# Kernel tuning notes

Hardware: AMD Instinct MI355X
Metric: run time of the kernel (lower is better)

Reference implementation:

```python
import jax, jax.numpy as jnp
import numpy as np

N_NODES = 100000
N_EDGES = 1600000
IN_FEATS = 512
HEADS = 8
HID = 8            # out_feats per head of the input layer
N_CLASSES = 40
NEG_SLOPE = 0.2    # DGL GATv2Conv default


def gatv2_layer(h, src, dst, Ws, bs, Wd, bd, attn, n_nodes):
    """One DGL-style GATv2Conv (eval mode: dropouts are identity).
    h: [N, F_in]; Ws/Wd: [F_in, H*D]; attn: [H, D]. Returns [N, H*D]."""
    H, D = attn.shape
    hs = (h @ Ws + bs).reshape(-1, H, D)   # fc_src(h)
    hd = (h @ Wd + bd).reshape(-1, H, D)   # fc_dst(h)
    es = hs[src]                           # [E,H,D] messages (feat_src on edges)
    ed = hd[dst]                           # [E,H,D]
    e = jax.nn.leaky_relu(es + ed, NEG_SLOPE)
    logits = jnp.einsum('ehd,hd->eh', e, attn)          # [E,H]
    # segment softmax over incoming edges of each dst node
    m = jax.ops.segment_max(logits, dst, num_segments=n_nodes)
    m = jnp.where(jnp.isfinite(m), m, 0.0)              # nodes with no in-edges
    p = jnp.exp(logits - m[dst])
    s = jax.ops.segment_sum(p, dst, num_segments=n_nodes)
    alpha = p / (s[dst] + 1e-9)                         # [E,H]
    out = jax.ops.segment_sum(alpha[:, :, None] * es, dst, num_segments=n_nodes)
    return out.reshape(n_nodes, H * D)


def setup_inputs() -> dict:
    key = jax.random.key(0)
    ks = jax.random.split(key, 12)
    x = jax.random.normal(ks[0], (N_NODES, IN_FEATS), dtype=jnp.float32)
    src = jax.random.randint(ks[1], (N_EDGES,), 0, N_NODES, dtype=jnp.int32)
    dst = jax.random.randint(ks[2], (N_EDGES,), 0, N_NODES, dtype=jnp.int32)
    s1 = 1.0 / np.sqrt(IN_FEATS)
    s2 = 1.0 / np.sqrt(HEADS * HID)
    W1s = jax.random.normal(ks[3], (IN_FEATS, HEADS * HID), dtype=jnp.float32) * s1
    W1d = jax.random.normal(ks[4], (IN_FEATS, HEADS * HID), dtype=jnp.float32) * s1
    b1s = jnp.zeros((HEADS * HID,), jnp.float32)
    b1d = jnp.zeros((HEADS * HID,), jnp.float32)
    a1 = jax.random.normal(ks[5], (HEADS, HID), dtype=jnp.float32) * s2
    W2s = jax.random.normal(ks[6], (HEADS * HID, N_CLASSES), dtype=jnp.float32) * s2
    W2d = jax.random.normal(ks[7], (HEADS * HID, N_CLASSES), dtype=jnp.float32) * s2
    b2s = jnp.zeros((N_CLASSES,), jnp.float32)
    b2d = jnp.zeros((N_CLASSES,), jnp.float32)
    a2 = jax.random.normal(ks[8], (1, N_CLASSES), dtype=jnp.float32) * (1.0 / np.sqrt(N_CLASSES))
    return {"x": x, "src": src, "dst": dst,
            "W1s": W1s, "b1s": b1s, "W1d": W1d, "b1d": b1d, "a1": a1,
            "W2s": W2s, "b2s": b2s, "W2d": W2d, "b2d": b2d, "a2": a2}


def reference(x, src, dst, W1s, b1s, W1d, b1d, a1, W2s, b2s, W2d, b2d, a2):
    h = gatv2_layer(x, src, dst, W1s, b1s, W1d, b1d, a1, N_NODES)   # [N, H*HID]
    h = jax.nn.elu(h)
    out = gatv2_layer(h, src, dst, W2s, b2s, W2d, b2d, a2, N_NODES)  # [N, C]
    return out
```

## Files before the change

kernel.cpp:

```cpp
#include <hip/hip_runtime.h>
#include <math.h>

#define N_NODES 100000
#define N_EDGES 1600000
#define F_IN    512
#define HD1     64
#define NHEAD   8
#define NC      40
#define NEG_SLOPE 0.2f

typedef _Float16 h8 __attribute__((ext_vector_type(8)));
typedef _Float16 h4 __attribute__((ext_vector_type(4)));
typedef float f4 __attribute__((ext_vector_type(4)));

__global__ __launch_bounds__(256) void prep_all(
    const float* __restrict__ W1s, const float* __restrict__ W1d,
    _Float16* __restrict__ btgf,
    const float* __restrict__ W2s, const float* __restrict__ W2d,
    _Float16* __restrict__ btg2, int* __restrict__ deg){
  int i = blockIdx.x*256 + threadIdx.x;
  {
    int j = i & 7, lane = (i>>3)&63, t = (i>>9)&7, kstep = i>>12;
    int k = kstep*32 + (lane>>4)*8 + j;
    int n = t*16 + (lane&15);
    float v = (n < 64) ? W1s[k*64 + n] : W1d[k*64 + (n-64)];
    btgf[i] = (_Float16)v;
  }
  if(i < 80*64){
    int n = i >> 6, k = i & 63;
    float v = (n < 40) ? W2s[k*40 + n] : W2d[k*40 + (n-40)];
    btg2[i] = (_Float16)v;
  }
  for(int k=i; k<N_NODES; k+=65536) deg[k] = 0;
}

__global__ __launch_bounds__(256,4) void gemm1_hist(
    const float* __restrict__ x, const _Float16* __restrict__ btgf,
    const float* __restrict__ bs, const float* __restrict__ bd,
    _Float16* __restrict__ hs, _Float16* __restrict__ hd,
    const int* __restrict__ dst, int* __restrict__ deg){
  __shared__ _Float16 at[2][64*136];
  int gid = blockIdx.x;
  int gdiv = gid/9;
  if(gid - gdiv*9 != 0){
    int hb = gid - gdiv - 1;
    int xcd = hb & 7;
    int lo = xcd*12500, hi = lo + 12500;
    int e0 = (hb >> 3)*1024 + threadIdx.x*4;
    if(e0 + 3 < N_EDGES){
      int4 d4 = *(const int4*)&dst[e0];
      if(d4.x >= lo && d4.x < hi) atomicAdd(&deg[d4.x], 1);
      if(d4.y >= lo && d4.y < hi) atomicAdd(&deg[d4.y], 1);
      if(d4.z >= lo && d4.z < hi) atomicAdd(&deg[d4.z], 1);
      if(d4.w >= lo && d4.w < hi) atomicAdd(&deg[d4.w], 1);
    } else {
      for(int j=0;j<4;j++){
        int e = e0 + j;
        if(e < N_EDGES){
          int d = dst[e];
          if(d >= lo && d < hi) atomicAdd(&deg[d], 1);
        }
      }
    }
    return;
  }
  int tid = threadIdx.x;
  int lane = tid & 63, w = tid >> 6;
  int l15 = lane & 15, quad = lane >> 4;
  int row0 = gdiv * 64;

  f4 acc[4][2];
  #pragma unroll
  for(int rt=0;rt<4;rt++){ acc[rt][0] = (f4){0.f,0.f,0.f,0.f}; acc[rt][1] = (f4){0.f,0.f,0.f,0.f}; }

  int sr[8], sc4[8];
  #pragma unroll
  for(int j=0;j<8;j++){
    int s = tid + j*256;
    int r = s >> 5, c4 = s & 31;
    int gr = row0 + r; if(gr >= N_NODES) gr = N_NODES-1;
    sr[j] = gr; sc4[j] = c4;
  }

  float4 pf[8];
  #pragma unroll
  for(int j=0;j<8;j++)
    pf[j] = *(const float4*)&x[sr[j]*F_IN + sc4[j]*4];

  for(int kc=0; kc<4; kc++){
    int buf = kc & 1;
    #pragma unroll
    for(int j=0;j<8;j++){
      int s = tid + j*256;
      int r = s >> 5, c4 = s & 31;
      h4 hv;
      hv[0]=(_Float16)pf[j].x; hv[1]=(_Float16)pf[j].y;
      hv[2]=(_Float16)pf[j].z; hv[3]=(_Float16)pf[j].w;
      *(h4*)&at[buf][r*136 + c4*4] = hv;
    }
    if(kc < 3){
      #pragma unroll
      for(int j=0;j<8;j++)
        pf[j] = *(const float4*)&x[sr[j]*F_IN + (kc+1)*128 + sc4[j]*4];
    }
    __syncthreads();
    #pragma unroll
    for(int ks=0;ks<4;ks++){
      int fbase = (((kc*4+ks)*8) + 2*w)*512 + lane*8;
      h8 b0 = *(const h8*)&btgf[fbase];
      h8 b1 = *(const h8*)&btgf[fbase + 512];
      #pragma unroll
      for(int rt=0;rt<4;rt++){
        h8 af = *(const h8*)&at[buf][(rt*16+l15)*136 + ks*32 + quad*8];
        acc[rt][0] = __builtin_amdgcn_mfma_f32_16x16x32_f16(af, b0, acc[rt][0], 0,0,0);
        acc[rt][1] = __builtin_amdgcn_mfma_f32_16x16x32_f16(af, b1, acc[rt][1], 0,0,0);
      }
    }
  }
  #pragma unroll
  for(int tt=0;tt<2;tt++){
    int colg = (2*w+tt)*16 + l15;
    float bv; _Float16* op; int c;
    if(colg < 64){ bv = bs[colg]; op = hs; c = colg; }
    else         { bv = bd[colg-64]; op = hd; c = colg-64; }
    #pragma unroll
    for(int rt=0;rt<4;rt++){
      #pragma unroll
      for(int reg=0;reg<4;reg++){
        int rr = row0 + rt*16 + quad*4 + reg;
        if(rr < N_NODES) op[rr*HD1 + c] = (_Float16)(acc[rt][tt][reg] + bv);
      }
    }
  }
}

__global__ __launch_bounds__(256) void scan1(const int* __restrict__ deg,
                                             int* __restrict__ row,
                                             int* __restrict__ bsum){
  __shared__ int sm[256];
  int t = threadIdx.x;
  int base = blockIdx.x*1024 + t*4;
  int v0 = base+0<N_NODES ? deg[base+0] : 0;
  int v1 = base+1<N_NODES ? deg[base+1] : 0;
  int v2 = base+2<N_NODES ? deg[base+2] : 0;
  int v3 = base+3<N_NODES ? deg[base+3] : 0;
  int tsum = v0+v1+v2+v3;
  sm[t] = tsum; __syncthreads();
  for(int off=1; off<256; off<<=1){
    int x = (t>=off) ? sm[t-off] : 0;
    __syncthreads();
    sm[t] += x;
    __syncthreads();
  }
  int excl = sm[t] - tsum;
  if(t==255) bsum[blockIdx.x] = sm[255];
  if(base+0<N_NODES) row[base+0] = excl;
  if(base+1<N_NODES) row[base+1] = excl+v0;
  if(base+2<N_NODES) row[base+2] = excl+v0+v1;
  if(base+3<N_NODES) row[base+3] = excl+v0+v1+v2;
}

#define SB_N 98
__global__ __launch_bounds__(256) void scan23(int* __restrict__ row,
                                              const int* __restrict__ bsum,
                                              int* __restrict__ cur){
  __shared__ int sm[128];
  __shared__ int sme[128];
  int t = threadIdx.x;
  int v = 0;
  if(t < 128){
    v = (t < SB_N) ? bsum[t] : 0;
    sm[t] = v;
  }
  __syncthreads();
  for(int off=1; off<128; off<<=1){
    int x = 0;
    if(t < 128 && t >= off) x = sm[t-off];
    __syncthreads();
    if(t < 128) sm[t] += x;
    __syncthreads();
  }
  if(t < 128) sme[t] = sm[t] - v;
  __syncthreads();
  int i = blockIdx.x*256 + t;
  if(i < N_NODES){
    int r = row[i] + sme[i>>10];
    row[i] = r; cur[i] = r;
  }
}

__global__ __launch_bounds__(256) void scatter_edges(const int* __restrict__ src,
                                                     const int* __restrict__ dst,
                                                     int* __restrict__ cur,
                                                     int* __restrict__ esrc){
  int xcd = blockIdx.x & 7;
  int lo = xcd*12500, hi = lo + 12500;
  int e0 = (blockIdx.x >> 3)*1024 + threadIdx.x*4;
  if(e0 + 3 < N_EDGES){
    int4 d4 = *(const int4*)&dst[e0];
    int4 s4 = *(const int4*)&src[e0];
    if(d4.x >= lo && d4.x < hi){ int p = atomicAdd(&cur[d4.x],1); esrc[p] = s4.x; }
    if(d4.y >= lo && d4.y < hi){ int p = atomicAdd(&cur[d4.y],1); esrc[p] = s4.y; }
    if(d4.z >= lo && d4.z < hi){ int p = atomicAdd(&cur[d4.z],1); esrc[p] = s4.z; }
    if(d4.w >= lo && d4.w < hi){ int p = atomicAdd(&cur[d4.w],1); esrc[p] = s4.w; }
  } else {
    for(int j=0;j<4;j++){
      int e = e0 + j;
      if(e < N_EDGES){
        int d = dst[e];
        if(d >= lo && d < hi){ int p = atomicAdd(&cur[d],1); esrc[p] = src[e]; }
      }
    }
  }
}

__global__ __launch_bounds__(256) void gemm2_mfma(
    const _Float16* __restrict__ h1h, const _Float16* __restrict__ btg,
    const float* __restrict__ bs, const float* __restrict__ bd,
    _Float16* __restrict__ hs2, _Float16* __restrict__ hd2){
  int tid = threadIdx.x;
  int lane = tid & 63, w = tid >> 6;
  int l15 = lane & 15, quad = lane >> 4;
  int rbase = blockIdx.x*192 + w*48;
  h8 bf[2][5];
  #pragma unroll
  for(int ks=0;ks<2;ks++)
    #pragma unroll
    for(int t=0;t<5;t++)
      bf[ks][t] = *(const h8*)&btg[(t*16 + l15)*64 + ks*32 + quad*8];
  f4 acc[3][5];
  #pragma unroll
  for(int mt=0;mt<3;mt++)
    #pragma unroll
    for(int t=0;t<5;t++) acc[mt][t] = (f4){0.f,0.f,0.f,0.f};
  #pragma unroll
  for(int mt=0;mt<3;mt++){
    int r = rbase + mt*16 + l15;
    if(r >= N_NODES) r = N_NODES-1;
    const _Float16* ap = h1h + r*HD1 + quad*8;
    #pragma unroll
    for(int ks=0;ks<2;ks++){
      h8 af = *(const h8*)(ap + ks*32);
      #pragma unroll
      for(int t=0;t<5;t++)
        acc[mt][t] = __builtin_amdgcn_mfma_f32_16x16x32_f16(af, bf[ks][t], acc[mt][t], 0,0,0);
    }
  }
  #pragma unroll
  for(int t=0;t<5;t++){
    int colg = t*16 + l15;
    float bv; _Float16* op; int c;
    if(colg < 40){ bv = bs[colg]; op = hs2; c = colg; }
    else         { bv = bd[colg-40]; op = hd2; c = colg-40; }
    #pragma unroll
    for(int mt=0;mt<3;mt++)
      #pragma unroll
      for(int reg=0;reg<4;reg++){
        int rr = rbase + mt*16 + quad*4 + reg;
        if(rr < N_NODES) op[rr*NC + c] = (_Float16)(acc[mt][t][reg] + bv);
      }
  }
}

__global__ __launch_bounds__(256) void node_attn1(
    const _Float16* __restrict__ hs, const _Float16* __restrict__ hd,
    const int* __restrict__ row, const int* __restrict__ deg,
    const int* __restrict__ esrc, const float* __restrict__ attn,
    _Float16* __restrict__ out){
  int node = blockIdx.x*4 + (threadIdx.x>>6);
  int lane = threadIdx.x & 63;
  if(node >= N_NODES) return;
  int h  = lane & 7;
  int es = lane >> 3;
  h8 hdh = *(const h8*)&hd[node*HD1 + h*8];
  float4 a0 = *(const float4*)&attn[h*8];
  float4 a1 = *(const float4*)&attn[h*8+4];
  float hdv[8], av[8];
  hdv[0]=(float)hdh[0]; hdv[1]=(float)hdh[1]; hdv[2]=(float)hdh[2]; hdv[3]=(float)hdh[3];
  hdv[4]=(float)hdh[4]; hdv[5]=(float)hdh[5]; hdv[6]=(float)hdh[6]; hdv[7]=(float)hdh[7];
  av[0]=a0.x; av[1]=a0.y; av[2]=a0.z; av[3]=a0.w;
  av[4]=a1.x; av[5]=a1.y; av[6]=a1.z; av[7]=a1.w;
  int st = row[node], dg = deg[node];
  float m = -1e30f, sum = 0.f;
  float acc[8] = {0.f,0.f,0.f,0.f,0.f,0.f,0.f,0.f};
  for(int sb = 0; sb < dg; sb += 64){
    int nblk = dg - sb; if(nblk > 64) nblk = 64;
    int li = st + sb + lane;
    int last = st + dg - 1;
    if(li > last) li = last;
    int sv = esrc[li];
    int iters = (nblk + 7) >> 3;
    int s0 = __shfl(sv, es);
    h8 hsh = *(const h8*)&hs[s0*HD1 + h*8];
    for(int i=0;i<iters;i++){
      h8 ch = hsh;
      bool val = (i*8 + es) < nblk;
      if(i+1 < iters){
        int sn = __shfl(sv, (i+1)*8 + es);
        hsh = *(const h8*)&hs[sn*HD1 + h*8];
      }
      float hsv[8]; float t = 0.f;
      #pragma unroll
      for(int j=0;j<8;j++){
        hsv[j] = (float)ch[j];
        float v = hsv[j] + hdv[j];
        v = fmaxf(v, NEG_SLOPE*v);
        t = fmaf(v, av[j], t);
      }
      if(!val) t = -1e30f;
      float mn = fmaxf(m, t);
      float eo = __expf(m - mn);
      float p  = __expf(t - mn);
      sum = sum*eo + p;
      #pragma unroll
      for(int j=0;j<8;j++) acc[j] = fmaf(p, hsv[j], acc[j]*eo);
      m = mn;
    }
  }
  float mg = m;
  mg = fmaxf(mg, __shfl_xor(mg,8));
  mg = fmaxf(mg, __shfl_xor(mg,16));
  mg = fmaxf(mg, __shfl_xor(mg,32));
  float sc = __expf(m - mg);
  sum *= sc;
  sum += __shfl_xor(sum,8); sum += __shfl_xor(sum,16); sum += __shfl_xor(sum,32);
  #pragma unroll
  for(int j=0;j<8;j++){
    acc[j] *= sc;
    acc[j] += __shfl_xor(acc[j],8);
    acc[j] += __shfl_xor(acc[j],16);
    acc[j] += __shfl_xor(acc[j],32);
  }
  if(es == 0){
    float inv = 1.f / (sum + 1e-9f);
    h8 o;
    #pragma unroll
    for(int j=0;j<8;j++){
      float r = acc[j] * inv;
      r = r>0.f ? r : expm1f(r);
      o[j] = (_Float16)r;
    }
    *(h8*)&out[node*HD1 + h*8] = o;
  }
}

__global__ __launch_bounds__(256) void node_attn2(
    const _Float16* __restrict__ hs, const _Float16* __restrict__ hd,
    const int* __restrict__ row, const int* __restrict__ deg,
    const int* __restrict__ esrc, const float* __restrict__ attn,
    float* __restrict__ out){
  int node = blockIdx.x*4 + (threadIdx.x>>6);
  int lane = threadIdx.x & 63;
  if(node >= N_NODES) return;
  int f  = lane & 7;
  int es = lane >> 3;
  bool fact = (f < 5);
  float hdv[8], av[8];
  if(fact){
    h8 hdh = *(const h8*)&hd[node*NC + f*8];
    float4 a0 = *(const float4*)&attn[f*8];
    float4 a1 = *(const float4*)&attn[f*8+4];
    hdv[0]=(float)hdh[0]; hdv[1]=(float)hdh[1]; hdv[2]=(float)hdh[2]; hdv[3]=(float)hdh[3];
    hdv[4]=(float)hdh[4]; hdv[5]=(float)hdh[5]; hdv[6]=(float)hdh[6]; hdv[7]=(float)hdh[7];
    av[0]=a0.x; av[1]=a0.y; av[2]=a0.z; av[3]=a0.w;
    av[4]=a1.x; av[5]=a1.y; av[6]=a1.z; av[7]=a1.w;
  } else {
    #pragma unroll
    for(int j=0;j<8;j++){ hdv[j]=0.f; av[j]=0.f; }
  }
  int st = row[node], dg = deg[node];
  float m = -1e30f, sum = 0.f;
  float acc[8] = {0.f,0.f,0.f,0.f,0.f,0.f,0.f,0.f};
  for(int sb = 0; sb < dg; sb += 64){
    int nblk = dg - sb; if(nblk > 64) nblk = 64;
    int li = st + sb + lane;
    int last = st + dg - 1;
    if(li > last) li = last;
    int sv = esrc[li];
    int iters = (nblk + 7) >> 3;
    int s0 = __shfl(sv, es);
    h8 hsh;
    if(fact) hsh = *(const h8*)&hs[s0*NC + f*8];
    for(int i=0;i<iters;i++){
      h8 ch = hsh;
      bool val = (i*8 + es) < nblk;
      int sn = 0;
      if(i+1 < iters) sn = __shfl(sv, (i+1)*8 + es);
      if(i+1 < iters && fact) hsh = *(const h8*)&hs[sn*NC + f*8];
      float hsv[8]; float t = 0.f;
      if(fact){
        #pragma unroll
        for(int j=0;j<8;j++){
          hsv[j] = (float)ch[j];
          float v = hsv[j] + hdv[j];
          v = fmaxf(v, NEG_SLOPE*v);
          t = fmaf(v, av[j], t);
        }
      } else {
        #pragma unroll
        for(int j=0;j<8;j++) hsv[j] = 0.f;
      }
      t += __shfl_xor(t,1); t += __shfl_xor(t,2); t += __shfl_xor(t,4);
      if(!val) t = -1e30f;
      float mn = fmaxf(m, t);
      float eo = __expf(m - mn);
      float p  = __expf(t - mn);
      sum = sum*eo + p;
      #pragma unroll
      for(int j=0;j<8;j++) acc[j] = fmaf(p, hsv[j], acc[j]*eo);
      m = mn;
    }
  }
  float mg = m;
  mg = fmaxf(mg, __shfl_xor(mg,8));
  mg = fmaxf(mg, __shfl_xor(mg,16));
  mg = fmaxf(mg, __shfl_xor(mg,32));
  float sc = __expf(m - mg);
  sum *= sc;
  sum += __shfl_xor(sum,8); sum += __shfl_xor(sum,16); sum += __shfl_xor(sum,32);
  #pragma unroll
  for(int j=0;j<8;j++){
    acc[j] *= sc;
    acc[j] += __shfl_xor(acc[j],8);
    acc[j] += __shfl_xor(acc[j],16);
    acc[j] += __shfl_xor(acc[j],32);
  }
  if(es == 0 && fact){
    float inv = 1.f / (sum + 1e-9f);
    f4 o0, o1;
    o0[0]=acc[0]*inv; o0[1]=acc[1]*inv; o0[2]=acc[2]*inv; o0[3]=acc[3]*inv;
    o1[0]=acc[4]*inv; o1[1]=acc[5]*inv; o1[2]=acc[6]*inv; o1[3]=acc[7]*inv;
    *(f4*)&out[node*NC + f*8]     = o0;
    *(f4*)&out[node*NC + f*8 + 4] = o1;
  }
}

extern "C" void kernel_launch(void* const* d_in, const int* in_sizes, int n_in,
                              void* d_out, int out_size, void* d_ws, size_t ws_size,
                              hipStream_t stream) {
  const float* x   = (const float*)d_in[0];
  const int*   src = (const int*)  d_in[1];
  const int*   dst = (const int*)  d_in[2];
  const float* W1s = (const float*)d_in[3];
  const float* b1s = (const float*)d_in[4];
  const float* W1d = (const float*)d_in[5];
  const float* b1d = (const float*)d_in[6];
  const float* a1  = (const float*)d_in[7];
  const float* W2s = (const float*)d_in[8];
  const float* b2s = (const float*)d_in[9];
  const float* W2d = (const float*)d_in[10];
  const float* b2d = (const float*)d_in[11];
  const float* a2  = (const float*)d_in[12];
  float* out = (float*)d_out;

  float* ws = (float*)d_ws;
  _Float16* hs1h = (_Float16*)ws;
  _Float16* hd1h = (_Float16*)(ws + 3200000);
  _Float16* h1h  = (_Float16*)(ws + 6400000);
  _Float16* hs2h = (_Float16*)(ws + 9600000);
  _Float16* hd2h = (_Float16*)(ws + 11600000);
  _Float16* btg1 = (_Float16*)(ws + 13600000);
  _Float16* btg2 = (_Float16*)(ws + 13632768);
  int*   deg  = (int*)(ws + 13635328);
  int*   row  = deg  + 100000;
  int*   cur  = row  + 100000;
  int*   bsum = cur  + 100000;
  int*   esrc = bsum + 128;

  dim3 b256(256);
  const int NB = (N_NODES+255)/256;
  const int SB = (N_NODES+1023)/1024;
  const int G1 = (N_NODES+63)/64;
  const int G2 = (N_NODES+191)/192;
  const int XB = ((N_EDGES+1023)/1024)*8;
  const int GH = G1 + XB;

  prep_all<<<256, b256, 0, stream>>>(W1s, W1d, btg1, W2s, W2d, btg2, deg);

  gemm1_hist<<<GH, b256, 0, stream>>>(x, btg1, b1s, b1d, hs1h, hd1h, dst, deg);

  scan1<<<SB, b256, 0, stream>>>(deg, row, bsum);
  scan23<<<NB, b256, 0, stream>>>(row, bsum, cur);
  scatter_edges<<<XB, b256, 0, stream>>>(src, dst, cur, esrc);

  node_attn1<<<(N_NODES+3)/4, b256, 0, stream>>>(hs1h, hd1h, row, deg, esrc, a1, h1h);

  gemm2_mfma<<<G2, b256, 0, stream>>>(h1h, btg2, b2s, b2d, hs2h, hd2h);
  node_attn2<<<(N_NODES+3)/4, b256, 0, stream>>>(hs2h, hd2h, row, deg, esrc, a2, out);
}
```

Baseline: 546.9 us.

## Split layer-1 GEMM in half and co-schedule halves with histogram and edge scatter

The first GEMM over node features is split into two kernels. The first half shares a launch with the degree histogram, and the second half shares a launch with the CSR edge scatter, which replaces the standalone scatter kernel. The aim is to hide the latency-bound atomic scatter work behind compute-heavy GEMM blocks, instead of running the scatter alone after the scans. GEMM and scatter blocks are interleaved in a 1:16 pattern. In exchange, the scatter kernel now carries the GEMM's LDS footprint and launch bounds, which may limit occupancy for the scatter blocks.

```diff
diff --git a/kernel.cpp b/kernel.cpp
--- a/kernel.cpp
+++ b/kernel.cpp
@@ -34,101 +34,147 @@
   for(int k=i; k<N_NODES; k+=65536) deg[k] = 0;
 }
 
-__global__ __launch_bounds__(256,4) void gemm1_hist(
+__device__ __forceinline__ void gemm1_body(
+    int row0, _Float16* at,
+    const float* __restrict__ x, const _Float16* __restrict__ btgf,
+    const float* __restrict__ bs, const float* __restrict__ bd,
+    _Float16* __restrict__ hs, _Float16* __restrict__ hd){
+  int tid = threadIdx.x;
+  int lane = tid & 63, w = tid >> 6;
+  int l15 = lane & 15, quad = lane >> 4;
+
+  f4 acc[4][2];
+  #pragma unroll
+  for(int rt=0;rt<4;rt++){ acc[rt][0] = (f4){0.f,0.f,0.f,0.f}; acc[rt][1] = (f4){0.f,0.f,0.f,0.f}; }
+
+  int sr[8], sc4[8];
+  #pragma unroll
+  for(int j=0;j<8;j++){
+    int s = tid + j*256;
+    int r = s >> 5, c4 = s & 31;
+    int gr = row0 + r; if(gr >= N_NODES) gr = N_NODES-1;
+    sr[j] = gr; sc4[j] = c4;
+  }
+
+  float4 pf[8];
+  #pragma unroll
+  for(int j=0;j<8;j++)
+    pf[j] = *(const float4*)&x[sr[j]*F_IN + sc4[j]*4];
+
+  for(int kc=0; kc<4; kc++){
+    _Float16* ab = at + (kc&1)*(64*136);
+    #pragma unroll
+    for(int j=0;j<8;j++){
+      int s = tid + j*256;
+      int r = s >> 5, c4 = s & 31;
+      h4 hv;
+      hv[0]=(_Float16)pf[j].x; hv[1]=(_Float16)pf[j].y;
+      hv[2]=(_Float16)pf[j].z; hv[3]=(_Float16)pf[j].w;
+      *(h4*)&ab[r*136 + c4*4] = hv;
+    }
+    if(kc < 3){
+      #pragma unroll
+      for(int j=0;j<8;j++)
+        pf[j] = *(const float4*)&x[sr[j]*F_IN + (kc+1)*128 + sc4[j]*4];
+    }
+    __syncthreads();
+    #pragma unroll
+    for(int ks=0;ks<4;ks++){
+      int fbase = (((kc*4+ks)*8) + 2*w)*512 + lane*8;
+      h8 b0 = *(const h8*)&btgf[fbase];
+      h8 b1 = *(const h8*)&btgf[fbase + 512];
+      #pragma unroll
+      for(int rt=0;rt<4;rt++){
+        h8 af = *(const h8*)&ab[(rt*16+l15)*136 + ks*32 + quad*8];
+        acc[rt][0] = __builtin_amdgcn_mfma_f32_16x16x32_f16(af, b0, acc[rt][0], 0,0,0);
+        acc[rt][1] = __builtin_amdgcn_mfma_f32_16x16x32_f16(af, b1, acc[rt][1], 0,0,0);
+      }
+    }
+  }
+  #pragma unroll
+  for(int tt=0;tt<2;tt++){
+    int colg = (2*w+tt)*16 + l15;
+    float bv; _Float16* op; int c;
+    if(colg < 64){ bv = bs[colg]; op = hs; c = colg; }
+    else         { bv = bd[colg-64]; op = hd; c = colg-64; }
+    #pragma unroll
+    for(int rt=0;rt<4;rt++){
+      #pragma unroll
+      for(int reg=0;reg<4;reg++){
+        int rr = row0 + rt*16 + quad*4 + reg;
+        if(rr < N_NODES) op[rr*HD1 + c] = (_Float16)(acc[rt][tt][reg] + bv);
+      }
+    }
+  }
+}
+
+#define G1A 782
+__global__ __launch_bounds__(256,4) void gemm1a_hist(
     const float* __restrict__ x, const _Float16* __restrict__ btgf,
     const float* __restrict__ bs, const float* __restrict__ bd,
     _Float16* __restrict__ hs, _Float16* __restrict__ hd,
     const int* __restrict__ dst, int* __restrict__ deg){
   __shared__ _Float16 at[2][64*136];
   int gid = blockIdx.x;
-  int gdiv = gid/9;
-  if(gid - gdiv*9 != 0){
-    int hb = gid - gdiv - 1;
-    int xcd = hb & 7;
-    int lo = xcd*12500, hi = lo + 12500;
-    int e0 = (hb >> 3)*1024 + threadIdx.x*4;
-    if(e0 + 3 < N_EDGES){
-      int4 d4 = *(const int4*)&dst[e0];
-      if(d4.x >= lo && d4.x < hi) atomicAdd(&deg[d4.x], 1);
-      if(d4.y >= lo && d4.y < hi) atomicAdd(&deg[d4.y], 1);
-      if(d4.z >= lo && d4.z < hi) atomicAdd(&deg[d4.z], 1);
-      if(d4.w >= lo && d4.w < hi) atomicAdd(&deg[d4.w], 1);
-    } else {
-      for(int j=0;j<4;j++){
-        int e = e0 + j;
-        if(e < N_EDGES){
-          int d = dst[e];
-          if(d >= lo && d < hi) atomicAdd(&deg[d], 1);
-        }
-      }
-    }
+  int gq = gid/17, gr = gid - gq*17;
+  if(gr==0 && gq < G1A){
+    gemm1_body(gq*64, &at[0][0], x, btgf, bs, bd, hs, hd);
     return;
   }
-  int tid = threadIdx.x;
-  int lane = tid & 63, w = tid >> 6;
-  int l15 = lane & 15, quad = lane >> 4;
-  int row0 = gdiv * 64;
-
-  f4 acc[4][2];
-  #pragma unroll
-  for(int rt=0;rt<4;rt++){ acc[rt][0] = (f4){0.f,0.f,0.f,0.f}; acc[rt][1] = (f4){0.f,0.f,0.f,0.f}; }
-
-  int sr[8], sc4[8];
-  #pragma unroll
-  for(int j=0;j<8;j++){
-    int s = tid + j*256;
-    int r = s >> 5, c4 = s & 31;
-    int gr = row0 + r; if(gr >= N_NODES) gr = N_NODES-1;
-    sr[j] = gr; sc4[j] = c4;
-  }
-
-  float4 pf[8];
-  #pragma unroll
-  for(int j=0;j<8;j++)
-    pf[j] = *(const float4*)&x[sr[j]*F_IN + sc4[j]*4];
-
-  for(int kc=0; kc<4; kc++){
-    int buf = kc & 1;
-    #pragma unroll
-    for(int j=0;j<8;j++){
-      int s = tid + j*256;
-      int r = s >> 5, c4 = s & 31;
-      h4 hv;
-      hv[0]=(_Float16)pf[j].x; hv[1]=(_Float16)pf[j].y;
-      hv[2]=(_Float16)pf[j].z; hv[3]=(_Float16)pf[j].w;
-      *(h4*)&at[buf][r*136 + c4*4] = hv;
-    }
-    if(kc < 3){
-      #pragma unroll
-      for(int j=0;j<8;j++)
-        pf[j] = *(const float4*)&x[sr[j]*F_IN + (kc+1)*128 + sc4[j]*4];
-    }
-    __syncthreads();
-    #pragma unroll
-    for(int ks=0;ks<4;ks++){
-      int fbase = (((kc*4+ks)*8) + 2*w)*512 + lane*8;
-      h8 b0 = *(const h8*)&btgf[fbase];
-      h8 b1 = *(const h8*)&btgf[fbase + 512];
-      #pragma unroll
-      for(int rt=0;rt<4;rt++){
-        h8 af = *(const h8*)&at[buf][(rt*16+l15)*136 + ks*32 + quad*8];
-        acc[rt][0] = __builtin_amdgcn_mfma_f32_16x16x32_f16(af, b0, acc[rt][0], 0,0,0);
-        acc[rt][1] = __builtin_amdgcn_mfma_f32_16x16x32_f16(af, b1, acc[rt][1], 0,0,0);
-      }
-    }
-  }
-  #pragma unroll
-  for(int tt=0;tt<2;tt++){
-    int colg = (2*w+tt)*16 + l15;
-    float bv; _Float16* op; int c;
-    if(colg < 64){ bv = bs[colg]; op = hs; c = colg; }
-    else         { bv = bd[colg-64]; op = hd; c = colg-64; }
-    #pragma unroll
-    for(int rt=0;rt<4;rt++){
-      #pragma unroll
-      for(int reg=0;reg<4;reg++){
-        int rr = row0 + rt*16 + quad*4 + reg;
-        if(rr < N_NODES) op[rr*HD1 + c] = (_Float16)(acc[rt][tt][reg] + bv);
+  int nm = gq + (gr?1:0); if(nm > G1A) nm = G1A;
+  int hb = gid - nm;
+  int xcd = hb & 7;
+  int lo = xcd*12500, hi = lo + 12500;
+  int e0 = (hb >> 3)*1024 + threadIdx.x*4;
+  if(e0 + 3 < N_EDGES){
+    int4 d4 = *(const int4*)&dst[e0];
+    if(d4.x >= lo && d4.x < hi) atomicAdd(&deg[d4.x], 1);
+    if(d4.y >= lo && d4.y < hi) atomicAdd(&deg[d4.y], 1);
+    if(d4.z >= lo && d4.z < hi) atomicAdd(&deg[d4.z], 1);
+    if(d4.w >= lo && d4.w < hi) atomicAdd(&deg[d4.w], 1);
+  } else {
+    for(int j=0;j<4;j++){
+      int e = e0 + j;
+      if(e < N_EDGES){
+        int d = dst[e];
+        if(d >= lo && d < hi) atomicAdd(&deg[d], 1);
+      }
+    }
+  }
+}
+
+#define G1B 781
+__global__ __launch_bounds__(256,4) void gemm1b_scatter(
+    const float* __restrict__ x, const _Float16* __restrict__ btgf,
+    const float* __restrict__ bs, const float* __restrict__ bd,
+    _Float16* __restrict__ hs, _Float16* __restrict__ hd,
+    const int* __restrict__ src, const int* __restrict__ dst,
+    int* __restrict__ cur, int* __restrict__ esrc){
+  __shared__ _Float16 at[2][64*136];
+  int gid = blockIdx.x;
+  int gq = gid/17, gr = gid - gq*17;
+  if(gr==0 && gq < G1B){
+    gemm1_body((G1A + gq)*64, &at[0][0], x, btgf, bs, bd, hs, hd);
+    return;
+  }
+  int nm = gq + (gr?1:0); if(nm > G1B) nm = G1B;
+  int hb = gid - nm;
+  int xcd = hb & 7;
+  int lo = xcd*12500, hi = lo + 12500;
+  int e0 = (hb >> 3)*1024 + threadIdx.x*4;
+  if(e0 + 3 < N_EDGES){
+    int4 d4 = *(const int4*)&dst[e0];
+    int4 s4 = *(const int4*)&src[e0];
+    if(d4.x >= lo && d4.x < hi){ int p = atomicAdd(&cur[d4.x],1); esrc[p] = s4.x; }
+    if(d4.y >= lo && d4.y < hi){ int p = atomicAdd(&cur[d4.y],1); esrc[p] = s4.y; }
+    if(d4.z >= lo && d4.z < hi){ int p = atomicAdd(&cur[d4.z],1); esrc[p] = s4.z; }
+    if(d4.w >= lo && d4.w < hi){ int p = atomicAdd(&cur[d4.w],1); esrc[p] = s4.w; }
+  } else {
+    for(int j=0;j<4;j++){
+      int e = e0 + j;
+      if(e < N_EDGES){
+        int d = dst[e];
+        if(d >= lo && d < hi){ int p = atomicAdd(&cur[d],1); esrc[p] = src[e]; }
       }
     }
   }
@@ -186,31 +232,6 @@
   if(i < N_NODES){
     int r = row[i] + sme[i>>10];
     row[i] = r; cur[i] = r;
-  }
-}
-
-__global__ __launch_bounds__(256) void scatter_edges(const int* __restrict__ src,
-                                                     const int* __restrict__ dst,
-                                                     int* __restrict__ cur,
-                                                     int* __restrict__ esrc){
-  int xcd = blockIdx.x & 7;
-  int lo = xcd*12500, hi = lo + 12500;
-  int e0 = (blockIdx.x >> 3)*1024 + threadIdx.x*4;
-  if(e0 + 3 < N_EDGES){
-    int4 d4 = *(const int4*)&dst[e0];
-    int4 s4 = *(const int4*)&src[e0];
-    if(d4.x >= lo && d4.x < hi){ int p = atomicAdd(&cur[d4.x],1); esrc[p] = s4.x; }
-    if(d4.y >= lo && d4.y < hi){ int p = atomicAdd(&cur[d4.y],1); esrc[p] = s4.y; }
-    if(d4.z >= lo && d4.z < hi){ int p = atomicAdd(&cur[d4.z],1); esrc[p] = s4.z; }
-    if(d4.w >= lo && d4.w < hi){ int p = atomicAdd(&cur[d4.w],1); esrc[p] = s4.w; }
-  } else {
-    for(int j=0;j<4;j++){
-      int e = e0 + j;
-      if(e < N_EDGES){
-        int d = dst[e];
-        if(d >= lo && d < hi){ int p = atomicAdd(&cur[d],1); esrc[p] = src[e]; }
-      }
-    }
   }
 }
 
@@ -470,18 +491,20 @@
   dim3 b256(256);
   const int NB = (N_NODES+255)/256;
   const int SB = (N_NODES+1023)/1024;
-  const int G1 = (N_NODES+63)/64;
   const int G2 = (N_NODES+191)/192;
   const int XB = ((N_EDGES+1023)/1024)*8;
-  const int GH = G1 + XB;
+  const int NA = G1A + XB;
+  const int NBk= G1B + XB;
 
   prep_all<<<256, b256, 0, stream>>>(W1s, W1d, btg1, W2s, W2d, btg2, deg);
 
-  gemm1_hist<<<GH, b256, 0, stream>>>(x, btg1, b1s, b1d, hs1h, hd1h, dst, deg);
+  gemm1a_hist<<<NA, b256, 0, stream>>>(x, btg1, b1s, b1d, hs1h, hd1h, dst, deg);
 
   scan1<<<SB, b256, 0, stream>>>(deg, row, bsum);
   scan23<<<NB, b256, 0, stream>>>(row, bsum, cur);
-  scatter_edges<<<XB, b256, 0, stream>>>(src, dst, cur, esrc);
+
+  gemm1b_scatter<<<NBk, b256, 0, stream>>>(x, btg1, b1s, b1d, hs1h, hd1h,
+                                           src, dst, cur, esrc);
 
   node_attn1<<<(N_NODES+3)/4, b256, 0, stream>>>(hs1h, hd1h, row, deg, esrc, a1, h1h);
 
```

After: 550.9 us. No clear change (+0.7%).
